# Optimization experiments

Measured on AMD Instinct MI355X. Metric: run time of the kernel, lower is better.

## Reference

```python
import jax, jax.numpy as jnp
import numpy as np

R = 3.9
EPS = 0.3
BETA = 0.15
STEPS = 15


def setup_inputs() -> dict:
    key = jax.random.key(0)
    k1, k2 = jax.random.split(key)
    drive = jax.random.uniform(k1, (2048, 1, 16384), dtype=jnp.float32)
    K = jnp.abs(jax.random.uniform(k2, (3,), dtype=jnp.float32))
    K = K / K.sum()
    return {"drive": drive, "K": K}


def reference(drive, K):
    # Circular 3-tap conv: torch conv1d is cross-correlation, padded circularly,
    # so local[i] = K[0]*m[i-1] + K[1]*m[i] + K[2]*m[i+1] (indices mod L).
    def step(grid, _):
        mapped = R * grid * (1.0 - grid)
        local = (K[0] * jnp.roll(mapped, 1, axis=-1)
                 + K[1] * mapped
                 + K[2] * jnp.roll(mapped, -1, axis=-1))
        physics = (1.0 - EPS) * mapped + EPS * local
        grid = (1.0 - BETA) * physics + BETA * drive
        return grid, None

    grid, _ = jax.lax.scan(step, drive, None, length=STEPS)
    return jnp.clip(grid, 0.0001, 1.0 - 0.0001)
```

## Files before the change

kernel.cpp:

```cpp
#include <hip/hip_runtime.h>
#include <stdint.h>


constexpr float Rc    = 3.9f;
constexpr float EPSc  = 0.3f;
constexpr float BETAc = 0.15f;
constexpr int   STEPS = 15;
constexpr int   L     = 16384;
constexpr int   CE    = 17;
constexpr int   SEG   = 1024;
constexpr int   GHOST = 32;
constexpr int   EXT   = SEG + 2*GHOST;
constexpr int   TPB   = 256;
constexpr int   WPB   = TPB / 64;
constexpr int   NBLK  = 1024;

constexpr int DPP_WAVE_SHL1 = 0x130;
constexpr int DPP_WAVE_SHR1 = 0x138;

__device__ __forceinline__ float dpp_shr1(float x) {
    return __int_as_float(__builtin_amdgcn_update_dpp(
        0, __float_as_int(x), DPP_WAVE_SHR1, 0xf, 0xf, true));
}
__device__ __forceinline__ float dpp_shl1(float x) {
    return __int_as_float(__builtin_amdgcn_update_dpp(
        0, __float_as_int(x), DPP_WAVE_SHL1, 0xf, 0xf, true));
}

typedef const __attribute__((address_space(1))) float gfloat;
typedef __attribute__((address_space(3))) float lfloat;

__global__ __launch_bounds__(TPB)
void cml1d_kernel(const float* __restrict__ drive,
                  const float* __restrict__ K,
                  float* __restrict__ out,
                  int T) {
    __shared__ float lds[WPB][2][EXT];

    const int lane = threadIdx.x & 63;
    const int wv   = threadIdx.x >> 6;
    const int gw0  = blockIdx.x * WPB + wv;

    const float K0 = K[0], K1 = K[1], K2 = K[2];
    const float A  = (1.0f - BETAc) * (1.0f - EPSc);
    const float B  = (1.0f - BETAc) * EPSc;
    const float d0 = Rc * (B * K0);
    const float d1 = Rc * (A + B * K1);
    const float d2 = Rc * (B * K2);

    float g[CE], bd[CE];

    auto prefetch = [&](int gw, float* buf) {
        const int row = gw >> 4, seg = gw & 15;
        const float* base = drive + (size_t)row * L;
        const int wb = seg * SEG - GHOST;
        #pragma unroll
        for (int j = 0; j < 4; ++j) {
            int idx = (wb + j * 256 + lane * 4) & (L - 1);
            __builtin_amdgcn_global_load_lds((gfloat*)(base + idx),
                                             (lfloat*)(buf + j * 256), 16, 0, 0);
        }
        int idx = (wb + 1024 + lane) & (L - 1);
        __builtin_amdgcn_global_load_lds((gfloat*)(base + idx),
                                         (lfloat*)(buf + 1024), 4, 0, 0);
    };
    auto unpack = [&](const float* buf) {
        #pragma unroll
        for (int i = 0; i < CE; ++i) {
            float v = buf[lane * CE + i];
            g[i]  = v;
            bd[i] = BETAc * v;
        }
    };

    prefetch(gw0, &lds[wv][0][0]);
    asm volatile("s_waitcnt vmcnt(0)" ::: "memory");
    unpack(&lds[wv][0][0]);

    int cur = 0;
    #pragma unroll 1
    for (int t = 0; t < T; ++t) {
        if (t < T - 1)
            prefetch((t + 1) * (NBLK * WPB) + gw0, &lds[wv][cur ^ 1][0]);
        __builtin_amdgcn_sched_barrier(0);

        for (int s = 0; s < STEPS; ++s) {
            float mh0  = fmaf(-g[0],      g[0],      g[0]);
            float mhT  = fmaf(-g[CE - 1], g[CE - 1], g[CE - 1]);
            float mleft  = dpp_shr1(mhT);
            float mright = dpp_shl1(mh0);

            float mprev = mh0;
            float mcur  = fmaf(-g[1], g[1], g[1]);
            const float m1s = mcur;
            float mTs = mcur;
            #pragma unroll
            for (int i = 1; i < CE - 1; ++i) {
                float mnext;
                if (i == CE - 2) { mnext = mhT; mTs = mcur; }
                else {
                    float gv = g[i + 1];
                    mnext = fmaf(-gv, gv, gv);
                }
                g[i] = fmaf(d0, mprev, fmaf(d1, mcur, fmaf(d2, mnext, bd[i])));
                mprev = mcur;
                mcur  = mnext;
            }
            g[0]      = fmaf(d0, mleft, fmaf(d1, mh0, fmaf(d2, m1s,    bd[0])));
            g[CE - 1] = fmaf(d0, mTs,   fmaf(d1, mhT, fmaf(d2, mright, bd[CE - 1])));
        }

        const int gw  = t * (NBLK * WPB) + gw0;
        const int row = gw >> 4, seg = gw & 15;
        float* tb = &lds[wv][cur][0];
        __builtin_amdgcn_wave_barrier();
        #pragma unroll
        for (int i = 0; i < CE; ++i) tb[lane * CE + i] = g[i];
        __builtin_amdgcn_wave_barrier();

        const float lo = 0.0001f;
        const float hi = 0.9999f;
        float* op = out + (size_t)row * L + seg * SEG;
        #pragma unroll
        for (int j = 0; j < 4; ++j) {
            int f = j * 64 + lane;
            float4 v = *reinterpret_cast<float4*>(&tb[GHOST + f * 4]);
            v.x = __builtin_amdgcn_fmed3f(v.x, lo, hi);
            v.y = __builtin_amdgcn_fmed3f(v.y, lo, hi);
            v.z = __builtin_amdgcn_fmed3f(v.z, lo, hi);
            v.w = __builtin_amdgcn_fmed3f(v.w, lo, hi);
            *reinterpret_cast<float4*>(op + f * 4) = v;
        }

        if (t < T - 1) {
            asm volatile("s_waitcnt vmcnt(4)" ::: "memory");
            unpack(&lds[wv][cur ^ 1][0]);
            cur ^= 1;
        }
    }
}

extern "C" void kernel_launch(void* const* d_in, const int* in_sizes, int n_in,
                              void* d_out, int out_size, void* d_ws, size_t ws_size,
                              hipStream_t stream) {
    const float* drive = (const float*)d_in[0];
    const float* K     = (const float*)d_in[1];
    float* out         = (float*)d_out;
    const int rows   = in_sizes[0] / L;
    const int gwaves = rows * (L / SEG);
    const int T      = gwaves / (NBLK * WPB);
    cml1d_kernel<<<dim3(NBLK), dim3(TPB), 0, stream>>>(drive, K, out, T);
}
```

Before: 233.9 us.

## Halve segment size, drop persistent loop, and use packed FP32 math

```diff
diff --git a/kernel.cpp b/kernel.cpp
--- a/kernel.cpp
+++ b/kernel.cpp
@@ -7,13 +7,15 @@
 constexpr float BETAc = 0.15f;
 constexpr int   STEPS = 15;
 constexpr int   L     = 16384;
-constexpr int   CE    = 17;
-constexpr int   SEG   = 1024;
+constexpr int   CE    = 9;
+constexpr int   HALF  = 4;
+constexpr int   NP    = HALF + 1;
+constexpr int   SEG   = 512;
 constexpr int   GHOST = 32;
 constexpr int   EXT   = SEG + 2*GHOST;
 constexpr int   TPB   = 256;
 constexpr int   WPB   = TPB / 64;
-constexpr int   NBLK  = 1024;
+constexpr int   SPR   = L / SEG;
 
 constexpr int DPP_WAVE_SHL1 = 0x130;
 constexpr int DPP_WAVE_SHR1 = 0x138;
@@ -27,19 +29,52 @@
         0, __float_as_int(x), DPP_WAVE_SHL1, 0xf, 0xf, true));
 }
 
+__device__ __forceinline__ float2 pk_mul(float2 a, float2 b) {
+    float2 d;
+    asm("v_pk_mul_f32 %0, %1, %2" : "=v"(d) : "v"(a), "v"(b));
+    return d;
+}
+__device__ __forceinline__ float2 pk_fma(float2 a, float2 b, float2 c) {
+    float2 d;
+    asm("v_pk_fma_f32 %0, %1, %2, %3" : "=v"(d) : "v"(a), "v"(b), "v"(c));
+    return d;
+}
+__device__ __forceinline__ float2 pk_fma_na(float2 a, float2 b, float2 c) {
+    float2 d;
+    asm("v_pk_fma_f32 %0, %1, %2, %3 neg_lo:[1,0,0] neg_hi:[1,0,0]"
+        : "=v"(d) : "v"(a), "v"(b), "v"(c));
+    return d;
+}
+
 typedef const __attribute__((address_space(1))) float gfloat;
 typedef __attribute__((address_space(3))) float lfloat;
 
-__global__ __launch_bounds__(TPB)
+__global__ __launch_bounds__(TPB, 8)
 void cml1d_kernel(const float* __restrict__ drive,
                   const float* __restrict__ K,
-                  float* __restrict__ out,
-                  int T) {
-    __shared__ float lds[WPB][2][EXT];
+                  float* __restrict__ out) {
+    __shared__ float lds[WPB][EXT];
 
     const int lane = threadIdx.x & 63;
     const int wv   = threadIdx.x >> 6;
-    const int gw0  = blockIdx.x * WPB + wv;
+    const int gw   = blockIdx.x * WPB + wv;
+    const int row  = gw >> 5;
+    const int seg  = gw & (SPR - 1);
+    const float* base = drive + (size_t)row * L;
+    const int wb = seg * SEG - GHOST;
+
+    float* buf = &lds[wv][0];
+    #pragma unroll
+    for (int j = 0; j < 2; ++j) {
+        int idx = (wb + j * 256 + lane * 4) & (L - 1);
+        __builtin_amdgcn_global_load_lds((gfloat*)(base + idx),
+                                         (lfloat*)(buf + j * 256), 16, 0, 0);
+    }
+    {
+        int idx = (wb + 512 + lane) & (L - 1);
+        __builtin_amdgcn_global_load_lds((gfloat*)(base + idx),
+                                         (lfloat*)(buf + 512), 4, 0, 0);
+    }
 
     const float K0 = K[0], K1 = K[1], K2 = K[2];
     const float A  = (1.0f - BETAc) * (1.0f - EPSc);
@@ -47,96 +82,59 @@
     const float d0 = Rc * (B * K0);
     const float d1 = Rc * (A + B * K1);
     const float d2 = Rc * (B * K2);
+    const float2 D0 = make_float2(d0, d0);
+    const float2 D1 = make_float2(d1, d1);
+    const float2 D2 = make_float2(d2, d2);
+    const float2 B2 = make_float2(BETAc, BETAc);
 
-    float g[CE], bd[CE];
+    asm volatile("s_waitcnt vmcnt(0)" ::: "memory");
 
-    auto prefetch = [&](int gw, float* buf) {
-        const int row = gw >> 4, seg = gw & 15;
-        const float* base = drive + (size_t)row * L;
-        const int wb = seg * SEG - GHOST;
+    float2 P[NP], BD[NP];
+    #pragma unroll
+    for (int j = 0; j < NP; ++j) {
+        P[j]  = make_float2(buf[lane * CE + j], buf[lane * CE + j + HALF]);
+        BD[j] = pk_mul(B2, P[j]);
+    }
+
+    for (int s = 0; s < STEPS; ++s) {
+        float2 MH[NP];
         #pragma unroll
-        for (int j = 0; j < 4; ++j) {
-            int idx = (wb + j * 256 + lane * 4) & (L - 1);
-            __builtin_amdgcn_global_load_lds((gfloat*)(base + idx),
-                                             (lfloat*)(buf + j * 256), 16, 0, 0);
+        for (int j = 0; j < NP; ++j)
+            MH[j] = pk_fma_na(P[j], P[j], P[j]);
+
+        const float mleft  = dpp_shr1(MH[NP - 1].y);
+        const float mright = dpp_shl1(MH[0].x);
+        const float2 MHm1_0 = make_float2(mleft, MH[HALF - 1].x);
+        const float2 MHp1_T = make_float2(MH[1].y, mright);
+
+        #pragma unroll
+        for (int j = 0; j < NP; ++j) {
+            float2 a = (j == 0)      ? MHm1_0 : MH[j - 1];
+            float2 b = (j == NP - 1) ? MHp1_T : MH[j + 1];
+            P[j] = pk_fma(D0, a, pk_fma(D1, MH[j], pk_fma(D2, b, BD[j])));
         }
-        int idx = (wb + 1024 + lane) & (L - 1);
-        __builtin_amdgcn_global_load_lds((gfloat*)(base + idx),
-                                         (lfloat*)(buf + 1024), 4, 0, 0);
-    };
-    auto unpack = [&](const float* buf) {
-        #pragma unroll
-        for (int i = 0; i < CE; ++i) {
-            float v = buf[lane * CE + i];
-            g[i]  = v;
-            bd[i] = BETAc * v;
-        }
-    };
+    }
 
-    prefetch(gw0, &lds[wv][0][0]);
-    asm volatile("s_waitcnt vmcnt(0)" ::: "memory");
-    unpack(&lds[wv][0][0]);
+    __builtin_amdgcn_wave_barrier();
+    #pragma unroll
+    for (int j = 0; j < NP; ++j) {
+        buf[lane * CE + j]        = P[j].x;
+        buf[lane * CE + j + HALF] = P[j].y;
+    }
+    __builtin_amdgcn_wave_barrier();
 
-    int cur = 0;
-    #pragma unroll 1
-    for (int t = 0; t < T; ++t) {
-        if (t < T - 1)
-            prefetch((t + 1) * (NBLK * WPB) + gw0, &lds[wv][cur ^ 1][0]);
-        __builtin_amdgcn_sched_barrier(0);
-
-        for (int s = 0; s < STEPS; ++s) {
-            float mh0  = fmaf(-g[0],      g[0],      g[0]);
-            float mhT  = fmaf(-g[CE - 1], g[CE - 1], g[CE - 1]);
-            float mleft  = dpp_shr1(mhT);
-            float mright = dpp_shl1(mh0);
-
-            float mprev = mh0;
-            float mcur  = fmaf(-g[1], g[1], g[1]);
-            const float m1s = mcur;
-            float mTs = mcur;
-            #pragma unroll
-            for (int i = 1; i < CE - 1; ++i) {
-                float mnext;
-                if (i == CE - 2) { mnext = mhT; mTs = mcur; }
-                else {
-                    float gv = g[i + 1];
-                    mnext = fmaf(-gv, gv, gv);
-                }
-                g[i] = fmaf(d0, mprev, fmaf(d1, mcur, fmaf(d2, mnext, bd[i])));
-                mprev = mcur;
-                mcur  = mnext;
-            }
-            g[0]      = fmaf(d0, mleft, fmaf(d1, mh0, fmaf(d2, m1s,    bd[0])));
-            g[CE - 1] = fmaf(d0, mTs,   fmaf(d1, mhT, fmaf(d2, mright, bd[CE - 1])));
-        }
-
-        const int gw  = t * (NBLK * WPB) + gw0;
-        const int row = gw >> 4, seg = gw & 15;
-        float* tb = &lds[wv][cur][0];
-        __builtin_amdgcn_wave_barrier();
-        #pragma unroll
-        for (int i = 0; i < CE; ++i) tb[lane * CE + i] = g[i];
-        __builtin_amdgcn_wave_barrier();
-
-        const float lo = 0.0001f;
-        const float hi = 0.9999f;
-        float* op = out + (size_t)row * L + seg * SEG;
-        #pragma unroll
-        for (int j = 0; j < 4; ++j) {
-            int f = j * 64 + lane;
-            float4 v = *reinterpret_cast<float4*>(&tb[GHOST + f * 4]);
-            v.x = __builtin_amdgcn_fmed3f(v.x, lo, hi);
-            v.y = __builtin_amdgcn_fmed3f(v.y, lo, hi);
-            v.z = __builtin_amdgcn_fmed3f(v.z, lo, hi);
-            v.w = __builtin_amdgcn_fmed3f(v.w, lo, hi);
-            *reinterpret_cast<float4*>(op + f * 4) = v;
-        }
-
-        if (t < T - 1) {
-            asm volatile("s_waitcnt vmcnt(4)" ::: "memory");
-            unpack(&lds[wv][cur ^ 1][0]);
-            cur ^= 1;
-        }
+    const float lo = 0.0001f;
+    const float hi = 0.9999f;
+    float* op = out + (size_t)row * L + seg * SEG;
+    #pragma unroll
+    for (int j = 0; j < 2; ++j) {
+        int f = j * 64 + lane;
+        float4 v = *reinterpret_cast<float4*>(&buf[GHOST + f * 4]);
+        v.x = __builtin_amdgcn_fmed3f(v.x, lo, hi);
+        v.y = __builtin_amdgcn_fmed3f(v.y, lo, hi);
+        v.z = __builtin_amdgcn_fmed3f(v.z, lo, hi);
+        v.w = __builtin_amdgcn_fmed3f(v.w, lo, hi);
+        *reinterpret_cast<float4*>(op + f * 4) = v;
     }
 }
 
@@ -147,7 +145,6 @@
     const float* K     = (const float*)d_in[1];
     float* out         = (float*)d_out;
     const int rows   = in_sizes[0] / L;
-    const int gwaves = rows * (L / SEG);
-    const int T      = gwaves / (NBLK * WPB);
-    cml1d_kernel<<<dim3(NBLK), dim3(TPB), 0, stream>>>(drive, K, out, T);
+    const int blocks = rows * SPR / WPB;
+    cml1d_kernel<<<dim3(blocks), dim3(TPB), 0, stream>>>(drive, K, out);
 }
```

Measured after the change: 232.7 us. About the same (-0.5%).
